# Performance work log

Hardware: AMD Instinct MI355X
Metric: run time of the kernel (lower is better)

## Reference

```python
import jax, jax.numpy as jnp
import numpy as np

N_ITERS = 3
EPS = 1e-5


def _ln(x, g, b):
    mu = jnp.mean(x, axis=-1, keepdims=True)
    var = jnp.mean((x - mu) ** 2, axis=-1, keepdims=True)
    return (x - mu) * jax.lax.rsqrt(var + EPS) * g + b


def setup_inputs() -> dict:
    key = jax.random.key(0)
    ks = iter(jax.random.split(key, 32))
    B, N, D_in, H, K = 128, 1024, 192, 128, 3

    def lin(o, i):
        w = (jax.random.normal(next(ks), (o, i)) / np.sqrt(i)).astype(jnp.float32)
        return w, jnp.zeros((o,), jnp.float32)

    Wp, bp = lin(H, D_in)
    Wq, bq = lin(H, H)
    Wk, bk = lin(H, H)
    Wv, bv = lin(H, H)
    Wih, bih = lin(3 * H, H)   # GRUCell input weights, stacked [r, z, n]
    Whh, bhh = lin(3 * H, H)   # GRUCell hidden weights
    W1, b1 = lin(2 * H, H)     # MLP expand
    W2, b2 = lin(H, 2 * H)     # MLP project
    ones = jnp.ones((H,), jnp.float32)
    zeros = jnp.zeros((H,), jnp.float32)

    return {
        "patch_tokens": jax.random.normal(next(ks), (B, N, D_in), jnp.float32),
        "noise": jax.random.normal(next(ks), (B, K, H), jnp.float32),
        "slot_mu": (jax.random.normal(next(ks), (1, K, H)) * 0.02).astype(jnp.float32),
        "slot_log_sigma": jnp.zeros((1, K, H), jnp.float32),
        "Wp": Wp, "bp": bp, "g_in": ones, "b_in": zeros,
        "Wq": Wq, "bq": bq, "Wk": Wk, "bk": bk, "Wv": Wv, "bv": bv,
        "Wih": Wih, "bih": bih, "Whh": Whh, "bhh": bhh,
        "g_s": ones, "b_s": zeros,
        "W1": W1, "b1": b1, "W2": W2, "b2": b2,
        "g_m": ones, "b_m": zeros,
    }


def reference(patch_tokens, noise, slot_mu, slot_log_sigma,
              Wp, bp, g_in, b_in,
              Wq, bq, Wk, bk, Wv, bv,
              Wih, bih, Whh, bhh,
              g_s, b_s, W1, b1, W2, b2, g_m, b_m):
    H = slot_mu.shape[-1]
    scale = 1.0 / jnp.sqrt(jnp.asarray(H, patch_tokens.dtype))

    # project + LayerNorm inputs once (k, v depend only on inputs -> hoisted)
    inputs = _ln(patch_tokens @ Wp.T + bp, g_in, b_in)      # (B, N, H)
    k = inputs @ Wk.T + bk                                  # (B, N, H)
    v = inputs @ Wv.T + bv                                  # (B, N, H)

    slots = slot_mu + jnp.exp(slot_log_sigma) * noise       # (B, K, H)

    def gru_cell(x, h):
        gi = x @ Wih.T + bih                                # (B, K, 3H)
        gh = h @ Whh.T + bhh
        ir, iz, inn = jnp.split(gi, 3, axis=-1)
        hr, hz, hn = jnp.split(gh, 3, axis=-1)
        r = jax.nn.sigmoid(ir + hr)
        z = jax.nn.sigmoid(iz + hz)
        n = jnp.tanh(inn + r * hn)
        return (1.0 - z) * n + z * h

    attn_weights = None
    for _ in range(N_ITERS):
        slots_prev = slots
        s = _ln(slots, g_s, b_s)
        q = s @ Wq.T + bq                                   # (B, K, H)
        attn = jnp.einsum('bkd,bnd->bkn', q, k) * scale     # (B, K, N)
        attn_weights = jax.nn.softmax(attn, axis=1)         # softmax over slots
        updates = jnp.einsum('bkn,bnd->bkd', attn_weights, v)
        slots = gru_cell(updates, slots_prev)
        h = _ln(slots, g_m, b_m)
        slots = slots + (jax.nn.gelu(h @ W1.T + b1, approximate=False) @ W2.T + b2)

    return slots, attn_weights
```

## Files before the change

### kernel.cpp

```cpp
#include <hip/hip_runtime.h>
#include <math.h>

constexpr float EPS = 1e-5f;
constexpr float SCALE = 0.08838834764831845f;

using f32x4  = __attribute__((ext_vector_type(4))) float;
using bf16x8 = __attribute__((ext_vector_type(8))) short;
using us8    = __attribute__((ext_vector_type(8))) unsigned short;

__device__ __forceinline__ unsigned short f2b_rne(float f) {
    unsigned int x = __float_as_uint(f);
    return (unsigned short)((x + 0x7fffu + ((x >> 16) & 1u)) >> 16);
}

__device__ __forceinline__ int swz32(int row, int k8) {
    int f = (row & 3) ^ ((row >> 2) & 3);
    return row * 32 + ((k8 ^ f) << 3);
}

__global__ __launch_bounds__(256) void prep_weights_kernel(
    const float* __restrict__ Wp, const float* __restrict__ Wk,
    const float* __restrict__ Wv, const float* __restrict__ Wih,
    const float* __restrict__ Whh, const float* __restrict__ W1,
    const float* __restrict__ W2, const float* __restrict__ Wq,
    unsigned short* __restrict__ hi, unsigned short* __restrict__ lo,
    float4* __restrict__ wt4)
{
    int idx = blockIdx.x * 256 + threadIdx.x;
    if (idx < 57344) {
        float v;
        if (idx < 24576)      v = Wp[idx];
        else if (idx < 40960) v = Wk[idx - 24576];
        else                  v = Wv[idx - 40960];
        unsigned int bits = __float_as_uint(v);
        hi[idx] = (unsigned short)(bits >> 16);
        lo[idx] = f2b_rne(v - __uint_as_float(bits & 0xffff0000u));
    } else {
        int li = idx - 57344;
        const float* src; int OUT, base, K;
        if (li < 12288)      { src = Wih; OUT = 384; base = 0;     K = 128; }
        else if (li < 24576) { src = Whh; OUT = 384; base = 12288; K = 128; }
        else if (li < 32768) { src = W1;  OUT = 256; base = 24576; K = 128; }
        else if (li < 40960) { src = W2;  OUT = 128; base = 32768; K = 256; }
        else                 { src = Wq;  OUT = 128; base = 40960; K = 128; }
        int lo2 = li - base;
        int kq = lo2 / OUT, t = lo2 - kq * OUT;
        float4 v;
        v.x = src[(size_t)t * K + 4 * kq];
        v.y = src[(size_t)t * K + 4 * kq + 1];
        v.z = src[(size_t)t * K + 4 * kq + 2];
        v.w = src[(size_t)t * K + 4 * kq + 3];
        wt4[li] = v;
    }
}

__global__ __launch_bounds__(256, 3) void fused_proj_kv_kernel(
    const float* __restrict__ patch,
    const unsigned short* __restrict__ Wphi, const unsigned short* __restrict__ Wplo,
    const unsigned short* __restrict__ Wkhi, const unsigned short* __restrict__ Wklo,
    const unsigned short* __restrict__ Wvhi, const unsigned short* __restrict__ Wvlo,
    const float* __restrict__ biasp, const float* __restrict__ g_in,
    const float* __restrict__ b_in, const float* __restrict__ biask,
    const float* __restrict__ biasv,
    float* __restrict__ kout, float* __restrict__ vout)
{
    __shared__ __align__(16) unsigned short mem[24576];

    const int tid  = threadIdx.x;
    const int lane = tid & 63, wave = tid >> 6;
    const int ln15 = lane & 15, quad = lane >> 4;
    const int bid  = blockIdx.x;
    const int m0   = ((bid & 7) * 256 + (bid >> 3)) * 64;

    const int wrow = wave * 16;
    f32x4 acc1[8];
#pragma unroll
    for (int nt = 0; nt < 8; nt++)
#pragma unroll
        for (int r = 0; r < 4; r++) acc1[nt][r] = 0.f;

    const int arow = tid >> 2, ak8 = tid & 3;
    const float* aptr = patch + (size_t)(m0 + arow) * 192 + ak8 * 8;
    float4 pa[6][2];
#pragma unroll
    for (int t6 = 0; t6 < 6; t6++) {
        pa[t6][0] = *(const float4*)(aptr + t6 * 32);
        pa[t6][1] = *(const float4*)(aptr + t6 * 32 + 4);
    }
    us8 pbh[2], pbl[2];
    int boff[2];
#pragma unroll
    for (int i = 0; i < 2; i++) {
        int c = tid + 256 * i;
        boff[i] = (c >> 2) * 192 + (c & 3) * 8;
        pbh[i] = *(const us8*)(Wphi + boff[i]);
        pbl[i] = *(const us8*)(Wplo + boff[i]);
    }

    const int ea = swz32(wrow + ln15, quad);

#pragma unroll
    for (int st = 0; st < 6; st++) {
        {
            float va[8] = {pa[st][0].x, pa[st][0].y, pa[st][0].z, pa[st][0].w,
                           pa[st][1].x, pa[st][1].y, pa[st][1].z, pa[st][1].w};
            us8 h, l;
#pragma unroll
            for (int j = 0; j < 8; j++) {
                unsigned int bits = __float_as_uint(va[j]);
                h[j] = (unsigned short)(bits >> 16);
                l[j] = f2b_rne(va[j] - __uint_as_float(bits & 0xffff0000u));
            }
            int e = swz32(arow, ak8);
            *(us8*)&mem[e]        = h;
            *(us8*)&mem[2048 + e] = l;
        }
#pragma unroll
        for (int i = 0; i < 2; i++) {
            int c = tid + 256 * i;
            int e = swz32(c >> 2, c & 3);
            *(us8*)&mem[4096 + e] = pbh[i];
            *(us8*)&mem[8192 + e] = pbl[i];
        }
        __syncthreads();

        if (st < 5) {
            int kn = (st + 1) * 32;
#pragma unroll
            for (int i = 0; i < 2; i++) {
                pbh[i] = *(const us8*)(Wphi + boff[i] + kn);
                pbl[i] = *(const us8*)(Wplo + boff[i] + kn);
            }
        }

        bf16x8 ah = *(const bf16x8*)&mem[ea];
        bf16x8 al = *(const bf16x8*)&mem[2048 + ea];
#pragma unroll
        for (int nt = 0; nt < 8; nt++) {
            int eb = swz32(nt * 16 + ln15, quad);
            bf16x8 bh = *(const bf16x8*)&mem[4096 + eb];
            bf16x8 bl = *(const bf16x8*)&mem[8192 + eb];
            acc1[nt] = __builtin_amdgcn_mfma_f32_16x16x32_bf16(ah, bh, acc1[nt], 0, 0, 0);
            acc1[nt] = __builtin_amdgcn_mfma_f32_16x16x32_bf16(ah, bl, acc1[nt], 0, 0, 0);
            acc1[nt] = __builtin_amdgcn_mfma_f32_16x16x32_bf16(al, bh, acc1[nt], 0, 0, 0);
        }
        __syncthreads();
    }

    us8 pw[4];
#pragma unroll
    for (int i = 0; i < 4; i++) {
        const unsigned short* pl = (i >> 1) ? Wklo : Wkhi;
        int c = tid + (i & 1) * 256;
        pw[i] = *(const us8*)(pl + (size_t)(c >> 2) * 128 + (c & 3) * 8);
    }

    {
        float bb[8], gg[8], be[8];
#pragma unroll
        for (int nt = 0; nt < 8; nt++) {
            int col = nt * 16 + ln15;
            bb[nt] = biasp[col]; gg[nt] = g_in[col]; be[nt] = b_in[col];
        }
#pragma unroll
        for (int nt = 0; nt < 8; nt++)
#pragma unroll
            for (int r = 0; r < 4; r++) acc1[nt][r] += bb[nt];

        float mu[4], rs[4];
#pragma unroll
        for (int r = 0; r < 4; r++) {
            float s = 0.f, s2 = 0.f;
#pragma unroll
            for (int nt = 0; nt < 8; nt++) {
                float v = acc1[nt][r];
                s += v; s2 += v * v;
            }
#pragma unroll
            for (int off = 1; off < 16; off <<= 1) {
                s  += __shfl_xor(s,  off, 64);
                s2 += __shfl_xor(s2, off, 64);
            }
            float m = s * (1.f / 128.f);
            mu[r] = m;
            rs[r] = rsqrtf(s2 * (1.f / 128.f) - m * m + EPS);
        }
#pragma unroll
        for (int nt = 0; nt < 8; nt++)
#pragma unroll
            for (int r = 0; r < 4; r++) {
                float v = (acc1[nt][r] - mu[r]) * rs[r] * gg[nt] + be[nt];
                int row = wrow + quad * 4 + r, col = nt * 16 + ln15;
                int xi = (row * 128 + col) ^ ((row & 7) << 3);
                unsigned int bits = __float_as_uint(v);
                mem[xi]        = (unsigned short)(bits >> 16);
                mem[8192 + xi] = f2b_rne(v - __uint_as_float(bits & 0xffff0000u));
            }
    }

    const int R  = (wave & 1) * 32;
    const int Cb = (wave >> 1) * 64;
    const int xorx = (ln15 & 7) << 3;

    float bbk[4], bbv[4];
#pragma unroll
    for (int nt = 0; nt < 4; nt++) {
        int col = Cb + nt * 16 + ln15;
        bbk[nt] = biask[col];
        bbv[nt] = biasv[col];
    }

    f32x4 acc[2][4];
#pragma unroll
    for (int mt = 0; mt < 2; mt++)
#pragma unroll
        for (int nt = 0; nt < 4; nt++)
#pragma unroll
            for (int r = 0; r < 4; r++) acc[mt][nt][r] = 0.f;

#pragma unroll
    for (int s = 0; s < 8; s++) {
#pragma unroll
        for (int i = 0; i < 4; i++) {
            int c = tid + (i & 1) * 256;
            int e = 16384 + (i >> 1) * 4096 + swz32(c >> 2, c & 3);
            *(us8*)&mem[e] = pw[i];
        }
        __syncthreads();

        if (s < 7) {
            int sn = s + 1, kkn = (sn & 3) * 32;
            const unsigned short* ph = (sn >> 2) ? Wvhi : Wkhi;
            const unsigned short* po = (sn >> 2) ? Wvlo : Wklo;
#pragma unroll
            for (int i = 0; i < 4; i++) {
                const unsigned short* pl = (i >> 1) ? po : ph;
                int c = tid + (i & 1) * 256;
                pw[i] = *(const us8*)(pl + (size_t)(c >> 2) * 128 + (c & 3) * 8 + kkn);
            }
        }

        int kk = (s & 3) * 32;
        bf16x8 xh[2], xl[2];
#pragma unroll
        for (int mt = 0; mt < 2; mt++) {
            int row = R + mt * 16 + ln15;
            int ei = (row * 128 + kk + quad * 8) ^ xorx;
            xh[mt] = *(const bf16x8*)&mem[ei];
            xl[mt] = *(const bf16x8*)&mem[8192 + ei];
        }
#pragma unroll
        for (int nt = 0; nt < 4; nt++) {
            int eb = 16384 + swz32(Cb + nt * 16 + ln15, quad);
            bf16x8 wh = *(const bf16x8*)&mem[eb];
            bf16x8 wl = *(const bf16x8*)&mem[4096 + eb];
#pragma unroll
            for (int mt = 0; mt < 2; mt++) {
                acc[mt][nt] = __builtin_amdgcn_mfma_f32_16x16x32_bf16(xh[mt], wh, acc[mt][nt], 0, 0, 0);
                acc[mt][nt] = __builtin_amdgcn_mfma_f32_16x16x32_bf16(xh[mt], wl, acc[mt][nt], 0, 0, 0);
                acc[mt][nt] = __builtin_amdgcn_mfma_f32_16x16x32_bf16(xl[mt], wh, acc[mt][nt], 0, 0, 0);
            }
        }

        if (s == 3) {
#pragma unroll
            for (int mt = 0; mt < 2; mt++)
#pragma unroll
                for (int nt = 0; nt < 4; nt++)
#pragma unroll
                    for (int r = 0; r < 4; r++) {
                        size_t o = (size_t)(m0 + R + mt * 16 + quad * 4 + r) * 128
                                 + Cb + nt * 16 + ln15;
                        kout[o] = acc[mt][nt][r] + bbk[nt];
                        acc[mt][nt][r] = 0.f;
                    }
        }
        if (s < 7) __syncthreads();
    }

#pragma unroll
    for (int mt = 0; mt < 2; mt++)
#pragma unroll
        for (int nt = 0; nt < 4; nt++)
#pragma unroll
            for (int r = 0; r < 4; r++) {
                size_t o = (size_t)(m0 + R + mt * 16 + quad * 4 + r) * 128
                         + Cb + nt * 16 + ln15;
                vout[o] = acc[mt][nt][r] + bbv[nt];
            }
}

__global__ __launch_bounds__(128) void init_lnq_kernel(
    const float* __restrict__ noise, const float* __restrict__ smu,
    const float* __restrict__ sls, const float* __restrict__ g_s,
    const float* __restrict__ b_s, const float4* __restrict__ WqT4,
    const float* __restrict__ bq, float* __restrict__ slots,
    float* __restrict__ q)
{
    __shared__ float s_l[128];
    __shared__ float red[4];
    const int row = blockIdx.x, tid = threadIdx.x;
    const int k = row % 3;
    float x = smu[k * 128 + tid] + expf(sls[k * 128 + tid]) * noise[row * 128 + tid];
    slots[row * 128 + tid] = x;

    float s = x, s2 = x * x;
#pragma unroll
    for (int off = 32; off >= 1; off >>= 1) {
        s += __shfl_down(s, off, 64); s2 += __shfl_down(s2, off, 64);
    }
    if ((tid & 63) == 0) { red[tid >> 6] = s; red[2 + (tid >> 6)] = s2; }
    __syncthreads();
    float S = red[0] + red[1], S2 = red[2] + red[3];
    float m = S * (1.f / 128.f);
    float r = rsqrtf(S2 * (1.f / 128.f) - m * m + EPS);
    s_l[tid] = (x - m) * r * g_s[tid] + b_s[tid];
    __syncthreads();

    float a = bq[tid];
#pragma unroll 8
    for (int kq = 0; kq < 32; kq++) {
        float4 w = WqT4[kq * 128 + tid];
        a += s_l[4 * kq] * w.x + s_l[4 * kq + 1] * w.y
           + s_l[4 * kq + 2] * w.z + s_l[4 * kq + 3] * w.w;
    }
    q[row * 128 + tid] = a;
}

__global__ __launch_bounds__(256) void attn_kernel(
    const float* __restrict__ q, const float* __restrict__ kbuf,
    const float* __restrict__ vbuf, float* __restrict__ upd_part,
    float* __restrict__ attn_out, int write_attn)
{
    __shared__ float q_l[3][132];
    __shared__ float lg[3][64];
    __shared__ float w_l[3][64];
    __shared__ float part[8][3][128];
    const int b = blockIdx.y, chunk = blockIdx.x, n0 = chunk * 64, tid = threadIdx.x;

    for (int idx = tid; idx < 384; idx += 256) {
        int s = idx >> 7, c = idx & 127;
        q_l[s][c + (c >> 5)] = q[b * 384 + idx];
    }

    const int tg = tid >> 5, d0 = (tid & 31) * 4;
    const float* vp = vbuf + ((size_t)b * 1024 + n0 + tg * 8) * 128 + d0;
    float4 vreg[8];
#pragma unroll
    for (int j = 0; j < 8; j++) vreg[j] = *(const float4*)(vp + (size_t)j * 128);

    const int n = tid >> 2, q4 = tid & 3;
    float4 kr[8];
    const float4* kg4 = (const float4*)(kbuf + ((size_t)b * 1024 + n0 + n) * 128 + q4 * 32);
#pragma unroll
    for (int i = 0; i < 8; i++) kr[i] = kg4[i];
    __syncthreads();

    {
        const float* q0 = &q_l[0][q4 * 33];
        const float* q1 = &q_l[1][q4 * 33];
        const float* q2 = &q_l[2][q4 * 33];
        float p0 = 0.f, p1 = 0.f, p2 = 0.f;
#pragma unroll
        for (int i = 0; i < 8; i++) {
            float kx[4] = {kr[i].x, kr[i].y, kr[i].z, kr[i].w};
#pragma unroll
            for (int j = 0; j < 4; j++) {
                float vv = kx[j];
                p0 += q0[4 * i + j] * vv;
                p1 += q1[4 * i + j] * vv;
                p2 += q2[4 * i + j] * vv;
            }
        }
        p0 += __shfl_xor(p0, 1, 64); p0 += __shfl_xor(p0, 2, 64);
        p1 += __shfl_xor(p1, 1, 64); p1 += __shfl_xor(p1, 2, 64);
        p2 += __shfl_xor(p2, 1, 64); p2 += __shfl_xor(p2, 2, 64);
        if (q4 == 0) {
            lg[0][n] = p0 * SCALE; lg[1][n] = p1 * SCALE; lg[2][n] = p2 * SCALE;
        }
    }
    __syncthreads();

    if (tid < 64) {
        float l0 = lg[0][tid], l1 = lg[1][tid], l2 = lg[2][tid];
        float m = fmaxf(l0, fmaxf(l1, l2));
        float e0 = expf(l0 - m), e1 = expf(l1 - m), e2 = expf(l2 - m);
        float inv = 1.f / (e0 + e1 + e2);
        w_l[0][tid] = e0 * inv; w_l[1][tid] = e1 * inv; w_l[2][tid] = e2 * inv;
        if (write_attn) {
            attn_out[b * 3072 + n0 + tid]        = e0 * inv;
            attn_out[b * 3072 + 1024 + n0 + tid] = e1 * inv;
            attn_out[b * 3072 + 2048 + n0 + tid] = e2 * inv;
        }
    }
    __syncthreads();

    {
        float4 a0 = {0.f, 0.f, 0.f, 0.f}, a1 = a0, a2 = a0;
#pragma unroll
        for (int j = 0; j < 8; j++) {
            float w0 = w_l[0][tg * 8 + j];
            float w1 = w_l[1][tg * 8 + j];
            float w2 = w_l[2][tg * 8 + j];
            float4 vv = vreg[j];
            a0.x += w0 * vv.x; a0.y += w0 * vv.y; a0.z += w0 * vv.z; a0.w += w0 * vv.w;
            a1.x += w1 * vv.x; a1.y += w1 * vv.y; a1.z += w1 * vv.z; a1.w += w1 * vv.w;
            a2.x += w2 * vv.x; a2.y += w2 * vv.y; a2.z += w2 * vv.z; a2.w += w2 * vv.w;
        }
        *(float4*)&part[tg][0][d0] = a0;
        *(float4*)&part[tg][1][d0] = a1;
        *(float4*)&part[tg][2][d0] = a2;
    }
    __syncthreads();

    for (int idx = tid; idx < 384; idx += 256) {
        int s = idx >> 7, d = idx & 127;
        float u = 0.f;
#pragma unroll
        for (int g = 0; g < 8; g++) u += part[g][s][d];
        upd_part[(((size_t)b * 16 + chunk) * 3 + s) * 128 + d] = u;
    }
}

__global__ __launch_bounds__(384) void gru_mlp_kernel(
    const float* __restrict__ slots_in, const float* __restrict__ upd_part,
    const float4* __restrict__ WihT4, const float* __restrict__ bih,
    const float4* __restrict__ WhhT4, const float* __restrict__ bhh,
    const float* __restrict__ g_m, const float* __restrict__ b_m,
    const float4* __restrict__ W1T4, const float* __restrict__ b1,
    const float4* __restrict__ W2T4, const float* __restrict__ b2,
    const float* __restrict__ g_s, const float* __restrict__ b_s,
    const float4* __restrict__ WqT4, const float* __restrict__ bq,
    float* __restrict__ slots_out, float* __restrict__ q_out, int write_q)
{
    __shared__ float u2[2][128];
    __shared__ float u_l[128], h_l[128];
    __shared__ float r_l[128], z_l[128], in_l[128], hn_l[128];
    __shared__ float n_l[128], hid_l[256], w2p[256];
    __shared__ float red[4];
    const int row = blockIdx.x, tid = threadIdx.x;
    const int bb_ = row / 3, ss = row - bb_ * 3;

    if (tid < 256) {
        int col = tid & 127, half = tid >> 7;
        const float* up = upd_part + (((size_t)bb_ * 16 + half * 8) * 3 + ss) * 128 + col;
        float u = 0.f;
#pragma unroll
        for (int c = 0; c < 8; c++) u += up[(size_t)c * 384];
        u2[half][col] = u;
        if (half == 0) h_l[col] = slots_in[row * 128 + col];
    }
    __syncthreads();
    if (tid < 128) u_l[tid] = u2[0][tid] + u2[1][tid];
    __syncthreads();

    {
        float gi = bih[tid], gh = bhh[tid];
#pragma unroll 8
        for (int kq = 0; kq < 32; kq++) {
            float4 a = WihT4[kq * 384 + tid];
            float4 c = WhhT4[kq * 384 + tid];
            gi += u_l[4 * kq] * a.x + u_l[4 * kq + 1] * a.y
                + u_l[4 * kq + 2] * a.z + u_l[4 * kq + 3] * a.w;
            gh += h_l[4 * kq] * c.x + h_l[4 * kq + 1] * c.y
                + h_l[4 * kq + 2] * c.z + h_l[4 * kq + 3] * c.w;
        }
        if (tid < 128)      r_l[tid] = 1.f / (1.f + expf(-(gi + gh)));
        else if (tid < 256) z_l[tid - 128] = 1.f / (1.f + expf(-(gi + gh)));
        else { in_l[tid - 256] = gi; hn_l[tid - 256] = gh; }
    }
    __syncthreads();

    float hnew = 0.f;
    if (tid < 128) {
        float nn = tanhf(in_l[tid] + r_l[tid] * hn_l[tid]);
        hnew = (1.f - z_l[tid]) * nn + z_l[tid] * h_l[tid];
        float s = hnew, s2 = hnew * hnew;
#pragma unroll
        for (int off = 32; off >= 1; off >>= 1) {
            s += __shfl_down(s, off, 64); s2 += __shfl_down(s2, off, 64);
        }
        if ((tid & 63) == 0) { red[tid >> 6] = s; red[2 + (tid >> 6)] = s2; }
    }
    __syncthreads();
    if (tid < 128) {
        float S = red[0] + red[1], S2 = red[2] + red[3];
        float m1 = S * (1.f / 128.f);
        float r1 = rsqrtf(S2 * (1.f / 128.f) - m1 * m1 + EPS);
        n_l[tid] = (hnew - m1) * r1 * g_m[tid] + b_m[tid];
    }
    __syncthreads();

    if (tid < 256) {
        float a = b1[tid];
#pragma unroll 8
        for (int kq = 0; kq < 32; kq++) {
            float4 w = W1T4[kq * 256 + tid];
            a += n_l[4 * kq] * w.x + n_l[4 * kq + 1] * w.y
               + n_l[4 * kq + 2] * w.z + n_l[4 * kq + 3] * w.w;
        }
        a = 0.5f * a * (1.f + erff(a * 0.70710678118654752f));
        hid_l[tid] = a;
    }
    __syncthreads();

    if (tid < 256) {
        int out = tid & 127, half = tid >> 7;
        float p = 0.f;
#pragma unroll 8
        for (int kq = half * 32; kq < half * 32 + 32; kq++) {
            float4 w = W2T4[kq * 128 + out];
            p += hid_l[4 * kq] * w.x + hid_l[4 * kq + 1] * w.y
               + hid_l[4 * kq + 2] * w.z + hid_l[4 * kq + 3] * w.w;
        }
        w2p[tid] = p;
    }
    __syncthreads();

    float snew = 0.f;
    if (tid < 128) {
        snew = hnew + b2[tid] + (w2p[tid] + w2p[128 + tid]);
        slots_out[row * 128 + tid] = snew;
    }

    if (write_q) {
        if (tid < 128) {
            float t1 = snew, t2 = snew * snew;
#pragma unroll
            for (int off = 32; off >= 1; off >>= 1) {
                t1 += __shfl_down(t1, off, 64); t2 += __shfl_down(t2, off, 64);
            }
            if ((tid & 63) == 0) { red[tid >> 6] = t1; red[2 + (tid >> 6)] = t2; }
        }
        __syncthreads();
        if (tid < 128) {
            float T = red[0] + red[1], T2 = red[2] + red[3];
            float m2 = T * (1.f / 128.f);
            float r2 = rsqrtf(T2 * (1.f / 128.f) - m2 * m2 + EPS);
            n_l[tid] = (snew - m2) * r2 * g_s[tid] + b_s[tid];
        }
        __syncthreads();
        if (tid < 256) {
            int out = tid & 127, half = tid >> 7;
            float p = (half == 0) ? bq[out] : 0.f;
#pragma unroll 8
            for (int kq = half * 16; kq < half * 16 + 16; kq++) {
                float4 w = WqT4[kq * 128 + out];
                p += n_l[4 * kq] * w.x + n_l[4 * kq + 1] * w.y
                   + n_l[4 * kq + 2] * w.z + n_l[4 * kq + 3] * w.w;
            }
            w2p[tid] = p;
        }
        __syncthreads();
        if (tid < 128) q_out[row * 128 + tid] = w2p[tid] + w2p[128 + tid];
    }
}

extern "C" void kernel_launch(void* const* d_in, const int* in_sizes, int n_in,
                              void* d_out, int out_size, void* d_ws, size_t ws_size,
                              hipStream_t stream)
{
    const float* patch   = (const float*)d_in[0];
    const float* noise   = (const float*)d_in[1];
    const float* slot_mu = (const float*)d_in[2];
    const float* slot_ls = (const float*)d_in[3];
    const float* Wp = (const float*)d_in[4];  const float* bp = (const float*)d_in[5];
    const float* g_in = (const float*)d_in[6]; const float* b_in = (const float*)d_in[7];
    const float* Wq = (const float*)d_in[8];  const float* bq = (const float*)d_in[9];
    const float* Wk = (const float*)d_in[10]; const float* bk = (const float*)d_in[11];
    const float* Wv = (const float*)d_in[12]; const float* bv = (const float*)d_in[13];
    const float* Wih = (const float*)d_in[14]; const float* bih = (const float*)d_in[15];
    const float* Whh = (const float*)d_in[16]; const float* bhh = (const float*)d_in[17];
    const float* g_s = (const float*)d_in[18]; const float* b_s = (const float*)d_in[19];
    const float* W1 = (const float*)d_in[20]; const float* b1 = (const float*)d_in[21];
    const float* W2 = (const float*)d_in[22]; const float* b2 = (const float*)d_in[23];
    const float* g_m = (const float*)d_in[24]; const float* b_m = (const float*)d_in[25];

    float* kbuf = (float*)d_ws;
    float* vbuf = kbuf + 16777216;
    unsigned short* w_hi = (unsigned short*)(vbuf + 16777216);
    unsigned short* w_lo = w_hi + 57344;
    unsigned short* wp_hi = w_hi,        * wp_lo = w_lo;
    unsigned short* wk_hi = w_hi + 24576,* wk_lo = w_lo + 24576;
    unsigned short* wv_hi = w_hi + 40960,* wv_lo = w_lo + 40960;
    float4* wt4 = (float4*)(w_lo + 57344);
    float4* wihT4 = wt4;
    float4* whhT4 = wt4 + 12288;
    float4* w1T4  = wt4 + 24576;
    float4* w2T4  = wt4 + 32768;
    float4* wqT4  = wt4 + 40960;
    float* slots = (float*)(wt4 + 45056);
    float* qbuf  = slots + 49152;
    float* part  = qbuf + 49152;

    float* out_slots = (float*)d_out;
    float* out_attn  = (float*)d_out + 49152;

    prep_weights_kernel<<<400, 256, 0, stream>>>(
        Wp, Wk, Wv, Wih, Whh, W1, W2, Wq, w_hi, w_lo, wt4);

    fused_proj_kv_kernel<<<2048, 256, 0, stream>>>(
        patch, wp_hi, wp_lo, wk_hi, wk_lo, wv_hi, wv_lo,
        bp, g_in, b_in, bk, bv, kbuf, vbuf);

    init_lnq_kernel<<<384, 128, 0, stream>>>(noise, slot_mu, slot_ls,
                                             g_s, b_s, wqT4, bq, slots, qbuf);

    for (int it = 0; it < 3; it++) {
        attn_kernel<<<dim3(16, 128), 256, 0, stream>>>(
            qbuf, kbuf, vbuf, part, out_attn, it == 2 ? 1 : 0);
        gru_mlp_kernel<<<384, 384, 0, stream>>>(
            slots, part, wihT4, bih, whhT4, bhh, g_m, b_m, w1T4, b1, w2T4, b2,
            g_s, b_s, wqT4, bq,
            (it == 2) ? out_slots : slots, qbuf, it == 2 ? 0 : 1);
    }
}
```

Before: 365.2 us.

## Process 256 tokens per attention block with double-buffered K/V register prefetch

Each attention block now covers 256 tokens instead of 64, looping over four sub-chunks and prefetching the next K or V tile into alternate register buffers while computing on the current one. This cuts the grid from 2048 to 512 blocks and shrinks the partial-update buffer, so the GRU kernel reduces 4 partials instead of 16. The cost is fewer blocks for latency hiding on a large GPU and much higher register pressure from four float4[8] arrays, which may reduce occupancy.

```diff
diff --git a/kernel.cpp b/kernel.cpp
--- a/kernel.cpp
+++ b/kernel.cpp
@@ -333,37 +333,44 @@
     float* __restrict__ attn_out, int write_attn)
 {
     __shared__ float q_l[3][132];
-    __shared__ float lg[3][64];
-    __shared__ float w_l[3][64];
+    __shared__ float lg[3][256];
+    __shared__ float w_l[3][256];
     __shared__ float part[8][3][128];
-    const int b = blockIdx.y, chunk = blockIdx.x, n0 = chunk * 64, tid = threadIdx.x;
+    const int b = blockIdx.y, chunk = blockIdx.x, n0 = chunk * 256, tid = threadIdx.x;
 
     for (int idx = tid; idx < 384; idx += 256) {
         int s = idx >> 7, c = idx & 127;
         q_l[s][c + (c >> 5)] = q[b * 384 + idx];
     }
 
+    const int n = tid >> 2, q4 = tid & 3;
+    const float4* kg4 = (const float4*)(kbuf + ((size_t)b * 1024 + n0 + n) * 128 + q4 * 32);
     const int tg = tid >> 5, d0 = (tid & 31) * 4;
     const float* vp = vbuf + ((size_t)b * 1024 + n0 + tg * 8) * 128 + d0;
-    float4 vreg[8];
-#pragma unroll
-    for (int j = 0; j < 8; j++) vreg[j] = *(const float4*)(vp + (size_t)j * 128);
-
-    const int n = tid >> 2, q4 = tid & 3;
-    float4 kr[8];
-    const float4* kg4 = (const float4*)(kbuf + ((size_t)b * 1024 + n0 + n) * 128 + q4 * 32);
-#pragma unroll
-    for (int i = 0; i < 8; i++) kr[i] = kg4[i];
-    __syncthreads();
-
-    {
-        const float* q0 = &q_l[0][q4 * 33];
-        const float* q1 = &q_l[1][q4 * 33];
-        const float* q2 = &q_l[2][q4 * 33];
+
+    float4 ka[8], kb2[8], va[8], vb2[8];
+#pragma unroll
+    for (int i = 0; i < 8; i++) ka[i] = kg4[i];
+    __syncthreads();
+
+    const float* q0 = &q_l[0][q4 * 33];
+    const float* q1 = &q_l[1][q4 * 33];
+    const float* q2 = &q_l[2][q4 * 33];
+#pragma unroll
+    for (int sc = 0; sc < 4; sc++) {
+        if (sc < 3) {
+            const float4* kn = kg4 + (size_t)(sc + 1) * 2048;
+#pragma unroll
+            for (int i = 0; i < 8; i++) ((sc & 1) ? ka : kb2)[i] = kn[i];
+        } else {
+#pragma unroll
+            for (int j = 0; j < 8; j++) va[j] = *(const float4*)(vp + (size_t)j * 128);
+        }
+        const float4* kc = (sc & 1) ? kb2 : ka;
         float p0 = 0.f, p1 = 0.f, p2 = 0.f;
 #pragma unroll
         for (int i = 0; i < 8; i++) {
-            float kx[4] = {kr[i].x, kr[i].y, kr[i].z, kr[i].w};
+            float kx[4] = {kc[i].x, kc[i].y, kc[i].z, kc[i].w};
 #pragma unroll
             for (int j = 0; j < 4; j++) {
                 float vv = kx[j];
@@ -376,41 +383,52 @@
         p1 += __shfl_xor(p1, 1, 64); p1 += __shfl_xor(p1, 2, 64);
         p2 += __shfl_xor(p2, 1, 64); p2 += __shfl_xor(p2, 2, 64);
         if (q4 == 0) {
-            lg[0][n] = p0 * SCALE; lg[1][n] = p1 * SCALE; lg[2][n] = p2 * SCALE;
-        }
-    }
-    __syncthreads();
-
-    if (tid < 64) {
+            lg[0][sc * 64 + n] = p0 * SCALE;
+            lg[1][sc * 64 + n] = p1 * SCALE;
+            lg[2][sc * 64 + n] = p2 * SCALE;
+        }
+    }
+    __syncthreads();
+
+    {
         float l0 = lg[0][tid], l1 = lg[1][tid], l2 = lg[2][tid];
         float m = fmaxf(l0, fmaxf(l1, l2));
         float e0 = expf(l0 - m), e1 = expf(l1 - m), e2 = expf(l2 - m);
         float inv = 1.f / (e0 + e1 + e2);
         w_l[0][tid] = e0 * inv; w_l[1][tid] = e1 * inv; w_l[2][tid] = e2 * inv;
         if (write_attn) {
-            attn_out[b * 3072 + n0 + tid]        = e0 * inv;
-            attn_out[b * 3072 + 1024 + n0 + tid] = e1 * inv;
-            attn_out[b * 3072 + 2048 + n0 + tid] = e2 * inv;
-        }
-    }
-    __syncthreads();
-
-    {
-        float4 a0 = {0.f, 0.f, 0.f, 0.f}, a1 = a0, a2 = a0;
+            int nn = n0 + tid;
+            attn_out[b * 3072 + nn]        = e0 * inv;
+            attn_out[b * 3072 + 1024 + nn] = e1 * inv;
+            attn_out[b * 3072 + 2048 + nn] = e2 * inv;
+        }
+    }
+    __syncthreads();
+
+    float4 a0 = {0.f, 0.f, 0.f, 0.f}, a1 = a0, a2 = a0;
+#pragma unroll
+    for (int sc = 0; sc < 4; sc++) {
+        if (sc < 3) {
+            const float* vn = vp + (size_t)(sc + 1) * 8192;
+#pragma unroll
+            for (int j = 0; j < 8; j++)
+                ((sc & 1) ? va : vb2)[j] = *(const float4*)(vn + (size_t)j * 128);
+        }
+        const float4* vc = (sc & 1) ? vb2 : va;
 #pragma unroll
         for (int j = 0; j < 8; j++) {
-            float w0 = w_l[0][tg * 8 + j];
-            float w1 = w_l[1][tg * 8 + j];
-            float w2 = w_l[2][tg * 8 + j];
-            float4 vv = vreg[j];
+            float w0 = w_l[0][sc * 64 + tg * 8 + j];
+            float w1 = w_l[1][sc * 64 + tg * 8 + j];
+            float w2 = w_l[2][sc * 64 + tg * 8 + j];
+            float4 vv = vc[j];
             a0.x += w0 * vv.x; a0.y += w0 * vv.y; a0.z += w0 * vv.z; a0.w += w0 * vv.w;
             a1.x += w1 * vv.x; a1.y += w1 * vv.y; a1.z += w1 * vv.z; a1.w += w1 * vv.w;
             a2.x += w2 * vv.x; a2.y += w2 * vv.y; a2.z += w2 * vv.z; a2.w += w2 * vv.w;
         }
-        *(float4*)&part[tg][0][d0] = a0;
-        *(float4*)&part[tg][1][d0] = a1;
-        *(float4*)&part[tg][2][d0] = a2;
-    }
+    }
+    *(float4*)&part[tg][0][d0] = a0;
+    *(float4*)&part[tg][1][d0] = a1;
+    *(float4*)&part[tg][2][d0] = a2;
     __syncthreads();
 
     for (int idx = tid; idx < 384; idx += 256) {
@@ -418,7 +436,7 @@
         float u = 0.f;
 #pragma unroll
         for (int g = 0; g < 8; g++) u += part[g][s][d];
-        upd_part[(((size_t)b * 16 + chunk) * 3 + s) * 128 + d] = u;
+        upd_part[(((size_t)b * 4 + chunk) * 3 + s) * 128 + d] = u;
     }
 }
 
@@ -443,10 +461,10 @@
 
     if (tid < 256) {
         int col = tid & 127, half = tid >> 7;
-        const float* up = upd_part + (((size_t)bb_ * 16 + half * 8) * 3 + ss) * 128 + col;
+        const float* up = upd_part + (((size_t)bb_ * 4 + half * 2) * 3 + ss) * 128 + col;
         float u = 0.f;
 #pragma unroll
-        for (int c = 0; c < 8; c++) u += up[(size_t)c * 384];
+        for (int c = 0; c < 2; c++) u += up[(size_t)c * 384];
         u2[half][col] = u;
         if (half == 0) h_l[col] = slots_in[row * 128 + col];
     }
@@ -607,7 +625,7 @@
                                              g_s, b_s, wqT4, bq, slots, qbuf);
 
     for (int it = 0; it < 3; it++) {
-        attn_kernel<<<dim3(16, 128), 256, 0, stream>>>(
+        attn_kernel<<<dim3(4, 128), 256, 0, stream>>>(
             qbuf, kbuf, vbuf, part, out_attn, it == 2 ? 1 : 0);
         gru_mlp_kernel<<<384, 384, 0, stream>>>(
             slots, part, wihT4, bih, whhT4, bhh, g_m, b_m, w1T4, b1, w2T4, b2,
```

Measured after the change: 358.9 us. Within noise of the previous version (-1.7%).
